# Performance work log

Measured on AMD Instinct MI355X. Metric: run time of the kernel, lower is better.

## Reference

```python
import jax, jax.numpy as jnp
import numpy as np
from math import sqrt

GAMMA = 2.0       # init gamma
SIGMA_G = 1.0     # init sigma (Gaussian prior width) -- NOT the forward `sigma` arg
ALPHA = 0.1       # prior mixing weight


def _hilbert_filter(L, dtype):
    h = np.zeros(L, dtype=np.float32)
    if L % 2 == 0:
        h[0] = h[L // 2] = 1.0
        h[1:L // 2] = 2.0
    else:
        h[0] = 1.0
        h[1:(L + 1) // 2] = 2.0
    return jnp.asarray(h)


def setup_inputs() -> dict:
    key = jax.random.key(0)
    ks = jax.random.split(key, 6)
    B, L, H, E = 4, 1024, 8, 64
    return {
        "q": jax.random.normal(ks[0], (B, L, H, E), jnp.float32),
        "k": jax.random.normal(ks[1], (B, L, H, E), jnp.float32),
        "v": jax.random.normal(ks[2], (B, L, H, E), jnp.float32),
        "sigma": jax.random.normal(ks[3], (B, L, H), jnp.float32),
        "hurst": jax.random.normal(ks[4], (B, L, H), jnpp if False else jnp.float32) if False else jax.random.normal(ks[4], (B, L, H), jnp.float32),
        "tau": jax.random.normal(ks[5], (B, L, H), jnp.float32),
    }


def reference(q, k, v, sigma, hurst, tau):
    B, L, H, E = q.shape
    scale = 1.0 / sqrt(E)

    # QK scores [B,H,L,L]. Note: original calls scores.masked_fill (non-inplace,
    # result discarded), so the causal mask has NO effect -- reproduced faithfully.
    scores = jnp.einsum('blhe,bshe->bhls', q, k)
    attn = scale * scores

    hurst_t = jax.nn.sigmoid(hurst) * 0.99 + 0.01          # [B,L,H]
    tau_t = jax.nn.sigmoid(tau) * 0.9 + 0.1                # [B,L,H]

    # fractal abscissa -> Gaussian prior [B,H,L,L]
    psi = jnp.cumsum(jnp.exp(GAMMA * hurst_t), axis=1)     # [B,L,H]
    diff = psi[:, :, None, :] - psi[:, None, :, :]          # [B,L,L,H]
    prior = jnp.exp(-diff ** 2 / (2.0 * SIGMA_G ** 2))
    prior = jnp.transpose(prior, (0, 3, 1, 2))              # [B,H,L,L]
    prior = prior / (jnp.sum(prior, axis=-1, keepdims=True) + 1e-6)

    # phase gate from Hilbert analytic signal of q-features
    x = jnp.transpose(q, (0, 2, 1, 3)).reshape(B, L, H * E)  # [B,L,C]
    sig = jnp.transpose(x, (0, 2, 1))                         # [B,C,L]
    hfilt = _hilbert_filter(L, sig.dtype)
    analytic = jnp.fft.ifft(jnp.fft.fft(sig, axis=-1) * hfilt[None, None, :], axis=-1)
    phase = jnp.arctan2(jnp.imag(analytic), jnp.real(analytic))  # [B,C,L]
    theta = jnp.arctan2(jnp.mean(jnp.sin(phase), axis=1),
                        jnp.mean(jnp.cos(phase), axis=1))        # [B,L]
    dphi = jnp.sin(0.5 * (theta[:, :, None] - theta[:, None, :]))  # [B,L,L]
    tau_d = jax.lax.stop_gradient(tau_t)                     # tau is detached
    S = jnp.exp(-dphi[..., None] ** 2 / (2.0 * tau_d[:, :, None, :] ** 2))  # [B,L,L,H]
    gate = jnp.transpose(S, (0, 3, 1, 2))                    # [B,H,L,L]

    prior = prior * gate
    prior = prior / (jnp.sum(prior, axis=-1, keepdims=True) + 1e-6)

    series = jax.nn.softmax(attn, axis=-1)                   # dropout p=0
    attn_combined = (1.0 - ALPHA) * series + ALPHA * prior
    V = jnp.einsum('bhls,bshd->blhd', attn_combined, v)      # [B,L,H,E]
    return V
```

## Files before the change

kernel.cpp:

```cpp
#include <hip/hip_runtime.h>
#include <hip/hip_bf16.h>
#include <math.h>

#define LL 1024
#define BB 4
#define HH 8
#define EE 64
#define CC (HH*EE)

typedef __attribute__((ext_vector_type(4))) float f32x4;
typedef __attribute__((ext_vector_type(8))) short bf16x8;
typedef __attribute__((ext_vector_type(4))) short bf16x4;

__device__ __forceinline__ unsigned short f2bf(float x) {
    unsigned u = __float_as_uint(x);
    u += 0x7FFFu + ((u >> 16) & 1u);
    return (unsigned short)(u >> 16);
}

__device__ __forceinline__ void dma16(const void* g, void* l) {
    typedef const __attribute__((address_space(1))) unsigned int* gup;
    typedef __attribute__((address_space(3))) unsigned int* lup;
    gup gp = (gup)(unsigned long long)g;
    lup lp = (lup)(unsigned int)(unsigned long long)l;
    __builtin_amdgcn_global_load_lds(gp, lp, 16, 0, 0);
}

__global__ __launch_bounds__(1024) void k_pre1(const float* __restrict__ hurst,
                                               const float* __restrict__ tau,
                                               const float* __restrict__ q,
                                               const float* __restrict__ kk,
                                               const float* __restrict__ vv,
                                               float* __restrict__ psi,
                                               float* __restrict__ taut,
                                               unsigned short* __restrict__ Agh,
                                               unsigned short* __restrict__ Agl,
                                               unsigned short* __restrict__ Xh,
                                               unsigned short* __restrict__ Xl,
                                               unsigned short* __restrict__ Qp,
                                               unsigned short* __restrict__ Kp,
                                               unsigned short* __restrict__ Vp) {
    __shared__ __align__(16) char smem[32768];
    int bid = blockIdx.x;
    int t = threadIdx.x;

    if (bid < 32) {
        float* sh = (float*)smem;
        int bh = bid;
        int b = bh >> 3, h = bh & 7;
        int l = t;
        float hu = hurst[((size_t)b * LL + l) * HH + h];
        float ht = 1.f / (1.f + expf(-hu)) * 0.99f + 0.01f;
        sh[l] = expf(2.0f * ht);
        __syncthreads();
        for (int off = 1; off < LL; off <<= 1) {
            float tmp = (l >= off) ? sh[l - off] : 0.f;
            __syncthreads();
            sh[l] += tmp;
            __syncthreads();
        }
        psi[((size_t)b * HH + h) * LL + l] = sh[l];
        float tv = tau[((size_t)b * LL + l) * HH + h];
        taut[((size_t)b * HH + h) * LL + l] = 1.f / (1.f + expf(-tv)) * 0.9f + 0.1f;
    } else if (bid < 288) {
        float* sh = (float*)smem;
        {
            int d = t;
            float vvv = 0.f;
            if (d & 1) {
                float a = 3.14159265358979323846f * (float)d / (float)LL;
                vvv = (2.0f / (float)LL) * (cosf(a) / sinf(a));
            }
            sh[d] = vvv;
        }
        __syncthreads();
        int bb = bid - 32;
        int im = bb >> 4, kt = bb & 15;
        if (t < 512) {
            int row = t >> 3, gr = t & 7;
            int i = im * 64 + row;
            bf16x8 hv, lv;
            #pragma unroll
            for (int j = 0; j < 8; ++j) {
                int kl = gr * 8 + j;
                float gg = sh[(i - kt * 64 - kl) & 1023];
                unsigned short hh = f2bf(gg);
                hv[j] = (short)hh;
                lv[j] = (short)f2bf(gg - __uint_as_float(((unsigned)hh) << 16));
            }
            size_t base = (size_t)bb * 4096;
            int pos = gr ^ (row & 7);
            *(bf16x8*)&Agh[base + row * 64 + pos * 8] = hv;
            *(bf16x8*)&Agl[base + row * 64 + pos * 8] = lv;
        }
    } else if (bid < 544) {
        int bb = bid - 288;
        int kt = bb >> 4, np = bb & 15;
        int bq = np >> 2;
        const float* qb = q + (size_t)bq * LL * CC;
        size_t base = (size_t)bb * 8192;
        int gid = t;
        int nl = gid & 15, nb = (gid >> 4) & 7, kg = gid >> 7;
        int e_n = np * 128 + nb * 16 + nl;
        int cy = (e_n >> 6) & 7;
        int e = e_n & 63;
        bf16x8 hv, lv;
        #pragma unroll
        for (int j = 0; j < 8; ++j) {
            int k2 = kt * 64 + kg * 8 + j;
            int l = ((k2 & 127) << 3) | cy;
            int h2 = k2 >> 7;
            float val = qb[l * 512 + h2 * 64 + e];
            unsigned short hh = f2bf(val);
            hv[j] = (short)hh;
            lv[j] = (short)f2bf(val - __uint_as_float(((unsigned)hh) << 16));
        }
        *(bf16x8*)&Xh[base + (size_t)gid * 8] = hv;
        *(bf16x8*)&Xl[base + (size_t)gid * 8] = lv;
    } else {
        int bb = bid - 544;
        int sub = t >> 8, tt = t & 255;
        int blk = bb * 4 + sub;
        int tile = blk & 15;
        int bh = blk >> 4;
        int h = bh & 7, b = bh >> 3;
        int l0 = tile * 64;
        unsigned short* vt = (unsigned short*)smem + sub * 4096;

        const float* qg = q + ((size_t)(b * LL + l0) * CC + (size_t)h * EE);
        const float* kg = kk + ((size_t)(b * LL + l0) * CC + (size_t)h * EE);
        const float* vg = vv + ((size_t)(b * LL + l0) * CC + (size_t)h * EE);
        unsigned short* Qo = Qp + ((size_t)bh * LL + l0) * 64;
        unsigned short* Ko = Kp + ((size_t)bh * LL + l0) * 64;
        unsigned short* Vo = Vp + ((size_t)bh * 16 + tile) * 4096;

        const float QS = 0.18033688011112042f;

        #pragma unroll
        for (int it = 0; it < 2; ++it) {
            int x = it * 256 + tt;
            int row = x >> 3, gr = x & 7;
            int pos = (gr ^ (row & 7)) * 8;
            const float* src = qg + (size_t)row * CC + gr * 8;
            float4 a4 = *(const float4*)src;
            float4 b4 = *(const float4*)(src + 4);
            bf16x8 o;
            o[0] = (short)f2bf(QS * a4.x); o[1] = (short)f2bf(QS * a4.y);
            o[2] = (short)f2bf(QS * a4.z); o[3] = (short)f2bf(QS * a4.w);
            o[4] = (short)f2bf(QS * b4.x); o[5] = (short)f2bf(QS * b4.y);
            o[6] = (short)f2bf(QS * b4.z); o[7] = (short)f2bf(QS * b4.w);
            *(bf16x8*)&Qo[row * 64 + pos] = o;
            src = kg + (size_t)row * CC + gr * 8;
            a4 = *(const float4*)src;
            b4 = *(const float4*)(src + 4);
            o[0] = (short)f2bf(a4.x); o[1] = (short)f2bf(a4.y);
            o[2] = (short)f2bf(a4.z); o[3] = (short)f2bf(a4.w);
            o[4] = (short)f2bf(b4.x); o[5] = (short)f2bf(b4.y);
            o[6] = (short)f2bf(b4.z); o[7] = (short)f2bf(b4.w);
            *(bf16x8*)&Ko[row * 64 + pos] = o;
        }

        #pragma unroll
        for (int it = 0; it < 4; ++it) {
            int x = it * 256 + tt;
            int s = x >> 4, i = x & 15;
            float4 a4 = *(const float4*)(vg + (size_t)s * CC + i * 4);
            int c = s >> 5, g4 = (s >> 2) & 3;
            int jj = ((s >> 4) & 1) * 4 + (s & 3);
            float vals[4] = {a4.x, a4.y, a4.z, a4.w};
            #pragma unroll
            for (int j2 = 0; j2 < 4; ++j2) {
                int e = i * 4 + j2;
                int ef = e >> 4, m16 = e & 15;
                vt[((((ef * 2 + c) * 4 + g4) * 16 + m16) * 8) + jj] = f2bf(vals[j2]);
            }
        }
        __syncthreads();
        #pragma unroll
        for (int it = 0; it < 2; ++it) {
            int x = it * 256 + tt;
            *(bf16x8*)&Vo[x * 8] = *(bf16x8*)&vt[x * 8];
        }
    }
}

__global__ __launch_bounds__(256) void k_hilb(const float* __restrict__ q,
                                              const unsigned short* __restrict__ Agh,
                                              const unsigned short* __restrict__ Agl,
                                              const unsigned short* __restrict__ Xh,
                                              const unsigned short* __restrict__ Xl,
                                              float* __restrict__ part_s,
                                              float* __restrict__ part_c) {
    __shared__ __align__(16) char smemB[98304];

    int t = threadIdx.x, lid = t & 63, wv = t >> 6;
    int m16 = lid & 15, g = lid >> 4;
    int wi = wv >> 1, wn = wv & 1;

    int bid = blockIdx.x;
    int xcd = bid & 7, o = bid >> 3;
    int im = ((xcd >> 2) << 3) + (o & 7);
    int np = ((xcd & 3) << 2) + (o >> 3);
    int i0 = im * 64, n0 = np * 128;
    int bq = np >> 2, quad = np & 3;
    const float* qb = q + (size_t)bq * LL * CC;

    const char* Ah_g = (const char*)Agh + (size_t)im * 16 * 8192;
    const char* Al_g = (const char*)Agl + (size_t)im * 16 * 8192;
    const char* Xh_g = (const char*)Xh;
    const char* Xl_g = (const char*)Xl;

#define AHOFF(bf) ((bf) * 49152)
#define ALOFF(bf) ((bf) * 49152 + 8192)
#define XHOFF(bf) ((bf) * 49152 + 16384)
#define XLOFF(bf) ((bf) * 49152 + 32768)
#define STAGE(bf, kt)                                                          \
    {                                                                          \
        size_t xb = ((size_t)(kt) * 16 + np) * 16384;                          \
        _Pragma("unroll")                                                      \
        for (int c = 0; c < 2; ++c) {                                          \
            int ch = wv + 4 * c;                                               \
            dma16(Ah_g + (kt) * 8192 + ch * 1024 + lid * 16,                   \
                  smemB + AHOFF(bf) + ch * 1024);                              \
            dma16(Al_g + (kt) * 8192 + ch * 1024 + lid * 16,                   \
                  smemB + ALOFF(bf) + ch * 1024);                              \
        }                                                                      \
        _Pragma("unroll")                                                      \
        for (int c = 0; c < 4; ++c) {                                          \
            int ch = wv + 4 * c;                                               \
            dma16(Xh_g + xb + ch * 1024 + lid * 16,                            \
                  smemB + XHOFF(bf) + ch * 1024);                              \
            dma16(Xl_g + xb + ch * 1024 + lid * 16,                            \
                  smemB + XLOFF(bf) + ch * 1024);                              \
        }                                                                      \
    }

    STAGE(0, 0);
    __syncthreads();

    f32x4 acc[2][4];
    #pragma unroll
    for (int mf = 0; mf < 2; ++mf)
        #pragma unroll
        for (int nf = 0; nf < 4; ++nf) acc[mf][nf] = (f32x4){0.f, 0.f, 0.f, 0.f};

    int cur = 0;
    for (int kt = 0; kt < 16; ++kt) {
        if (kt < 15) {
            STAGE(cur ^ 1, kt + 1);
            asm volatile("s_waitcnt vmcnt(12)" ::: "memory");
        } else {
            asm volatile("s_waitcnt vmcnt(0)" ::: "memory");
        }
        __builtin_amdgcn_sched_barrier(0);
        __builtin_amdgcn_s_barrier();
        asm volatile("" ::: "memory");

        const unsigned short* AhL = (const unsigned short*)(smemB + AHOFF(cur));
        const unsigned short* AlL = (const unsigned short*)(smemB + ALOFF(cur));
        const unsigned short* XhL = (const unsigned short*)(smemB + XHOFF(cur));
        const unsigned short* XlL = (const unsigned short*)(smemB + XLOFF(cur));

        __builtin_amdgcn_s_setprio(1);
        #pragma unroll
        for (int s = 0; s < 2; ++s) {
            bf16x8 Ahf[2], Alf[2];
            #pragma unroll
            for (int mf = 0; mf < 2; ++mf) {
                int row = wi * 32 + 16 * mf + m16;
                int pos = (s * 4 + g) ^ (m16 & 7);
                Ahf[mf] = *(bf16x8*)&AhL[row * 64 + pos * 8];
                Alf[mf] = *(bf16x8*)&AlL[row * 64 + pos * 8];
            }
            #pragma unroll
            for (int nf = 0; nf < 4; ++nf) {
                int nb = wn * 4 + nf;
                int goff = (((s * 4 + g) * 8 + nb) * 16 + m16) * 8;
                bf16x8 Bh = *(bf16x8*)&XhL[goff];
                bf16x8 Bl = *(bf16x8*)&XlL[goff];
                #pragma unroll
                for (int mf = 0; mf < 2; ++mf) {
                    acc[mf][nf] = __builtin_amdgcn_mfma_f32_16x16x32_bf16(Ahf[mf], Bh, acc[mf][nf], 0, 0, 0);
                    acc[mf][nf] = __builtin_amdgcn_mfma_f32_16x16x32_bf16(Ahf[mf], Bl, acc[mf][nf], 0, 0, 0);
                    acc[mf][nf] = __builtin_amdgcn_mfma_f32_16x16x32_bf16(Alf[mf], Bh, acc[mf][nf], 0, 0, 0);
                }
            }
        }
        __builtin_amdgcn_s_setprio(0);

        asm volatile("" ::: "memory");
        __builtin_amdgcn_s_barrier();
        cur ^= 1;
    }

    float svacc[2][4], cvacc[2][4];
    #pragma unroll
    for (int mf = 0; mf < 2; ++mf)
        #pragma unroll
        for (int r = 0; r < 4; ++r) { svacc[mf][r] = 0.f; cvacc[mf][r] = 0.f; }

    #pragma unroll
    for (int mf = 0; mf < 2; ++mf) {
        #pragma unroll
        for (int nf = 0; nf < 4; ++nf) {
            #pragma unroll
            for (int r = 0; r < 4; ++r) {
                float iv = acc[mf][nf][r];
                int ig = i0 + wi * 32 + 16 * mf + 4 * g + r;
                int ng = n0 + wn * 64 + 16 * nf + m16;
                int cc2 = ng & 511;
                int cy = cc2 >> 6, e = cc2 & 63;
                int l = ((ig & 127) << 3) | cy;
                int h2 = ig >> 7;
                float re = qb[l * 512 + h2 * 64 + e];
                float rr = sqrtf(re * re + iv * iv);
                float sv, cv;
                if (rr > 0.f) { sv = iv / rr; cv = re / rr; }
                else { sv = 0.f; cv = 1.f; }
                svacc[mf][r] += sv;
                cvacc[mf][r] += cv;
            }
        }
    }
    __syncthreads();
    float* psv = (float*)smemB;
    float* pcv = (float*)(smemB + 512);
    #pragma unroll
    for (int mf = 0; mf < 2; ++mf) {
        #pragma unroll
        for (int r = 0; r < 4; ++r) {
            float s = svacc[mf][r], c = cvacc[mf][r];
            s += __shfl_xor(s, 1); s += __shfl_xor(s, 2);
            s += __shfl_xor(s, 4); s += __shfl_xor(s, 8);
            c += __shfl_xor(c, 1); c += __shfl_xor(c, 2);
            c += __shfl_xor(c, 4); c += __shfl_xor(c, 8);
            if (m16 == 0) {
                psv[wv * 32 + 16 * mf + 4 * g + r] = s;
                pcv[wv * 32 + 16 * mf + 4 * g + r] = c;
            }
        }
    }
    __syncthreads();
    if (t < 64) {
        int wg = (t >> 5) * 2;
        float s = psv[wg * 32 + (t & 31)] + psv[(wg + 1) * 32 + (t & 31)];
        float c = pcv[wg * 32 + (t & 31)] + pcv[(wg + 1) * 32 + (t & 31)];
        size_t oidx = ((size_t)bq * 1024 + (i0 + t)) * 4 + quad;
        part_s[oidx] = s;
        part_c[oidx] = c;
    }
#undef AHOFF
#undef ALOFF
#undef XHOFF
#undef XLOFF
#undef STAGE
}

__global__ __launch_bounds__(1024) void k_pcs(const float* __restrict__ psi,
                                              const float* __restrict__ taut,
                                              const float* __restrict__ part_s,
                                              const float* __restrict__ part_c,
                                              float* __restrict__ pcs) {
    int tid = blockIdx.x * 1024 + threadIdx.x;
    int bh = tid >> 10, l = tid & 1023;
    int b = bh >> 3;
    float ss = 0.f, cc2 = 0.f;
    size_t pbase = ((size_t)b * 1024 + l) * 4;
    #pragma unroll
    for (int qd = 0; qd < 4; ++qd) {
        ss += part_s[pbase + qd];
        cc2 += part_c[pbase + qd];
    }
    float r2 = ss * ss + cc2 * cc2;
    float cth = 1.f, sth = 0.f;
    if (r2 > 0.f) {
        float rn = rsqrtf(r2);
        cth = cc2 * rn; sth = ss * rn;
    }
    float ta = taut[tid];
    float4 o;
    o.x = psi[tid] * 0.8493218003f;
    o.y = cth;
    o.z = sth;
    o.w = 0.3606737602f / (ta * ta);
    *(float4*)&pcs[(size_t)tid * 4] = o;
}

__global__ __launch_bounds__(256, 3) void k_attn(const unsigned short* __restrict__ Qp,
                                                 const unsigned short* __restrict__ Kp,
                                                 const unsigned short* __restrict__ Vp,
                                                 const float* __restrict__ pcs,
                                                 float* __restrict__ out) {
    __shared__ __align__(16) char smemB[43008];

    int t = threadIdx.x;
    int lid = t & 63;
    int wv = t >> 6;
    int m16 = lid & 15;
    int g = lid >> 4;

    int bid = blockIdx.x;
    int blk = (bid & 7) * 64 + (bid >> 3);
    int qt = blk & 15;
    int bh = blk >> 4;
    int h = bh & 7, b = bh >> 3;
    int l0 = qt * 64;

    const char* Qg = (const char*)(Qp + ((size_t)bh * LL + l0) * 64);
    const char* Kg = (const char*)(Kp + (size_t)bh * LL * 64);
    const char* Vg = (const char*)(Vp + (size_t)bh * LL * 64);
    const float* pcsg = pcs + (size_t)bh * LL * 4;

    int qrow = wv * 16 + m16;
    float4 myq = *(const float4*)&pcsg[(size_t)(l0 + qrow) * 4];
    float psiq = myq.x, cq = myq.y, sq = myq.z;
    float wgt = myq.w, nwgt = -myq.w;

#define KOFF(bf) (8192 + (bf) * 8192)
#define VOFF(bf) (24576 + (bf) * 8192)
#define POFF(bf) (40960 + (bf) * 1024)
#define STAGE(bf, tile)                                                        \
    {                                                                          \
        const char* kb8 = Kg + (tile) * 8192;                                  \
        const char* vb8 = Vg + (tile) * 8192;                                  \
        _Pragma("unroll")                                                      \
        for (int c = 0; c < 2; ++c) {                                          \
            int ch = wv + 4 * c;                                               \
            dma16(kb8 + ch * 1024 + lid * 16, smemB + KOFF(bf) + ch * 1024);   \
            dma16(vb8 + ch * 1024 + lid * 16, smemB + VOFF(bf) + ch * 1024);   \
        }                                                                      \
        dma16((const char*)pcsg + (tile) * 1024 + lid * 16, smemB + POFF(bf)); \
    }

    #pragma unroll
    for (int c = 0; c < 2; ++c) {
        int ch = wv + 4 * c;
        dma16(Qg + ch * 1024 + lid * 16, smemB + ch * 1024);
    }
    STAGE(0, 0);
    __syncthreads();

    const unsigned short* qlds = (const unsigned short*)smemB;
    bf16x8 qf[2];
    #pragma unroll
    for (int ec = 0; ec < 2; ++ec) {
        int pos = (4 * ec + g) ^ (m16 & 7);
        qf[ec] = *(bf16x8*)&qlds[(wv * 16 + m16) * 64 + pos * 8];
    }

    f32x4 accS[4], accP[4];
    #pragma unroll
    for (int f = 0; f < 4; ++f) {
        accS[f] = (f32x4){0.f, 0.f, 0.f, 0.f};
        accP[f] = (f32x4){0.f, 0.f, 0.f, 0.f};
    }
    float ssel = 0.f, spgl = 0.f;
    int cur = 0;

    for (int tile = 0; tile < 16; ++tile) {
        if (tile < 15) {
            STAGE(cur ^ 1, tile + 1);
            asm volatile("s_waitcnt vmcnt(5)" ::: "memory");
        } else {
            asm volatile("s_waitcnt vmcnt(0)" ::: "memory");
        }
        __builtin_amdgcn_sched_barrier(0);
        __builtin_amdgcn_s_barrier();
        asm volatile("" ::: "memory");

        const unsigned short* kbuf = (const unsigned short*)(smemB + KOFF(cur));
        const unsigned short* vbuf = (const unsigned short*)(smemB + VOFF(cur));
        const float* pcb = (const float*)(smemB + POFF(cur));

        f32x4 st[4];
        #pragma unroll
        for (int f = 0; f < 4; ++f) st[f] = (f32x4){0.f, 0.f, 0.f, 0.f};
        __builtin_amdgcn_s_setprio(1);
        #pragma unroll
        for (int ec = 0; ec < 2; ++ec) {
            int pos = (4 * ec + g) ^ (m16 & 7);
            #pragma unroll
            for (int f = 0; f < 4; ++f) {
                bf16x8 ka = *(bf16x8*)&kbuf[(16 * f + m16) * 64 + pos * 8];
                st[f] = __builtin_amdgcn_mfma_f32_16x16x32_bf16(ka, qf[ec], st[f], 0, 0, 0);
            }
        }
        __builtin_amdgcn_s_setprio(0);

        float psum = 0.f;
        float ps_[16], pg_[16];
        #pragma unroll
        for (int f = 0; f < 4; ++f) {
            #pragma unroll
            for (int r = 0; r < 4; ++r) {
                float4 pc4 = *(const float4*)&pcb[(16 * f + 4 * g + r) * 4];
                float p = exp2f(st[f][r]);
                psum += p;
                float d = psiq - pc4.x;
                float cd = fmaf(cq, pc4.y, sq * pc4.z);
                float arg = fmaf(-d, d, fmaf(wgt, cd, nwgt));
                float pgv = exp2f(arg);
                spgl += pgv;
                ps_[f * 4 + r] = p;
                pg_[f * 4 + r] = pgv;
            }
        }
        ssel += psum;

        union PK8 { unsigned w[8]; bf16x8 v[2]; } SS, GG;
        #pragma unroll
        for (int i2 = 0; i2 < 8; ++i2) {
            __hip_bfloat162 hs = __float22bfloat162_rn(
                make_float2(ps_[2 * i2], ps_[2 * i2 + 1]));
            __hip_bfloat162 hg = __float22bfloat162_rn(
                make_float2(pg_[2 * i2], pg_[2 * i2 + 1]));
            unsigned ws2, wg2;
            __builtin_memcpy(&ws2, &hs, 4);
            __builtin_memcpy(&wg2, &hg, 4);
            SS.w[i2] = ws2;
            GG.w[i2] = wg2;
        }

        __builtin_amdgcn_s_setprio(1);
        #pragma unroll
        for (int c = 0; c < 2; ++c) {
            #pragma unroll
            for (int ef = 0; ef < 4; ++ef) {
                bf16x8 vb = *(bf16x8*)&vbuf[(((ef * 2 + c) * 4 + g) * 16 + m16) * 8];
                accS[ef] = __builtin_amdgcn_mfma_f32_16x16x32_bf16(SS.v[c], vb, accS[ef], 0, 0, 0);
                accP[ef] = __builtin_amdgcn_mfma_f32_16x16x32_bf16(GG.v[c], vb, accP[ef], 0, 0, 0);
            }
        }
        __builtin_amdgcn_s_setprio(0);

        asm volatile("" ::: "memory");
        __builtin_amdgcn_s_barrier();
        cur ^= 1;
    }

    ssel += __shfl_xor(ssel, 16); ssel += __shfl_xor(ssel, 32);
    spgl += __shfl_xor(spgl, 16); spgl += __shfl_xor(spgl, 32);
    float cs = 0.9f / ssel;
    float cp = 0.1f / (spgl + 1e-6f);
    float* ob = out + ((size_t)(b * LL + l0 + wv * 16) * CC + (size_t)h * EE);
    #pragma unroll
    for (int r = 0; r < 4; ++r) {
        float csr = __shfl(cs, 4 * g + r);
        float cpr = __shfl(cp, 4 * g + r);
        #pragma unroll
        for (int f = 0; f < 4; ++f) {
            ob[(size_t)(4 * g + r) * CC + 16 * f + m16] =
                csr * accS[f][r] + cpr * accP[f][r];
        }
    }
#undef KOFF
#undef VOFF
#undef POFF
#undef STAGE
}

extern "C" void kernel_launch(void* const* d_in, const int* in_sizes, int n_in,
                              void* d_out, int out_size, void* d_ws, size_t ws_size,
                              hipStream_t stream) {
    const float* q = (const float*)d_in[0];
    const float* k = (const float*)d_in[1];
    const float* v = (const float*)d_in[2];
    const float* hurst = (const float*)d_in[4];
    const float* tau = (const float*)d_in[5];
    float* out = (float*)d_out;

    float* ws = (float*)d_ws;
    float* gi     = ws;
    float* psi    = gi + LL;
    float* taut   = psi + (size_t)BB * HH * LL;
    float* costh  = taut + (size_t)BB * HH * LL;
    float* sinth  = costh + (size_t)BB * LL;
    float* part_s = sinth + (size_t)BB * LL;
    float* part_c = part_s + (size_t)BB * LL * 4;
    float* pcs    = part_c + (size_t)BB * LL * 4;
    unsigned short* Qp = (unsigned short*)(pcs + (size_t)BB * HH * LL * 4);
    unsigned short* Kp = Qp + (size_t)BB * HH * LL * 64;
    unsigned short* Vp = Kp + (size_t)BB * HH * LL * 64;
    unsigned short* Agh = Vp + (size_t)BB * HH * LL * 64;
    unsigned short* Agl = Agh + (size_t)1048576;
    unsigned short* Xh  = (unsigned short*)d_out;
    unsigned short* Xl  = Xh + (size_t)2097152;

    k_pre1<<<672, 1024, 0, stream>>>(hurst, tau, q, k, v, psi, taut,
                                     Agh, Agl, Xh, Xl, Qp, Kp, Vp);
    k_hilb<<<256, 256, 0, stream>>>(q, Agh, Agl, Xh, Xl, part_s, part_c);
    k_pcs<<<32, 1024, 0, stream>>>(psi, taut, part_s, part_c, pcs);
    k_attn<<<BB * HH * (LL / 64), 256, 0, stream>>>(Qp, Kp, Vp, pcs, out);
}
```

Baseline: 80.32 us.

## Halve Hilbert GEMM N-tile to double grid, and stage two key tiles per attention step

The Hilbert DFT GEMM kernel now uses 64-column output tiles instead of 128, launching 512 blocks with smaller shared buffers so more of the GPU is occupied. Its partial sin/cos sums are split eight ways instead of four, and the reduction kernel reads eight partials. The attention kernel now stages 128 keys per pipeline step (two 64-key subtiles), halving barrier and wait overhead. It also loads Q fragments straight from global memory into registers and drops the occupancy hint. The larger shared-memory footprint may lower attention occupancy, and the Hilbert A-matrix is loaded twice as often across blocks.

```diff
diff --git a/kernel.cpp b/kernel.cpp
--- a/kernel.cpp
+++ b/kernel.cpp
@@ -191,7 +191,7 @@
                                               const unsigned short* __restrict__ Xl,
                                               float* __restrict__ part_s,
                                               float* __restrict__ part_c) {
-    __shared__ __align__(16) char smemB[98304];
+    __shared__ __align__(16) char smemB[65536];
 
     int t = threadIdx.x, lid = t & 63, wv = t >> 6;
     int m16 = lid & 15, g = lid >> 4;
@@ -199,10 +199,11 @@
 
     int bid = blockIdx.x;
     int xcd = bid & 7, o = bid >> 3;
-    int im = ((xcd >> 2) << 3) + (o & 7);
-    int np = ((xcd & 3) << 2) + (o >> 3);
-    int i0 = im * 64, n0 = np * 128;
-    int bq = np >> 2, quad = np & 3;
+    int im  = ((xcd >> 2) << 3) + (o & 7);
+    int np8 = ((xcd & 3) << 3) + (o >> 3);
+    int i0 = im * 64, n0 = np8 * 64;
+    int bq = np8 >> 3, oct = np8 & 7;
+    int np = np8 >> 1, nb0 = (np8 & 1) * 4;
     const float* qb = q + (size_t)bq * LL * CC;
 
     const char* Ah_g = (const char*)Agh + (size_t)im * 16 * 8192;
@@ -210,10 +211,10 @@
     const char* Xh_g = (const char*)Xh;
     const char* Xl_g = (const char*)Xl;
 
-#define AHOFF(bf) ((bf) * 49152)
-#define ALOFF(bf) ((bf) * 49152 + 8192)
-#define XHOFF(bf) ((bf) * 49152 + 16384)
-#define XLOFF(bf) ((bf) * 49152 + 32768)
+#define AHOFF(bf) ((bf) * 32768)
+#define ALOFF(bf) ((bf) * 32768 + 8192)
+#define XHOFF(bf) ((bf) * 32768 + 16384)
+#define XLOFF(bf) ((bf) * 32768 + 24576)
 #define STAGE(bf, kt)                                                          \
     {                                                                          \
         size_t xb = ((size_t)(kt) * 16 + np) * 16384;                          \
@@ -224,13 +225,9 @@
                   smemB + AHOFF(bf) + ch * 1024);                              \
             dma16(Al_g + (kt) * 8192 + ch * 1024 + lid * 16,                   \
                   smemB + ALOFF(bf) + ch * 1024);                              \
-        }                                                                      \
-        _Pragma("unroll")                                                      \
-        for (int c = 0; c < 4; ++c) {                                          \
-            int ch = wv + 4 * c;                                               \
-            dma16(Xh_g + xb + ch * 1024 + lid * 16,                            \
+            dma16(Xh_g + xb + (ch * 8 + nb0) * 256 + lid * 16,                 \
                   smemB + XHOFF(bf) + ch * 1024);                              \
-            dma16(Xl_g + xb + ch * 1024 + lid * 16,                            \
+            dma16(Xl_g + xb + (ch * 8 + nb0) * 256 + lid * 16,                 \
                   smemB + XLOFF(bf) + ch * 1024);                              \
         }                                                                      \
     }
@@ -238,17 +235,17 @@
     STAGE(0, 0);
     __syncthreads();
 
-    f32x4 acc[2][4];
+    f32x4 acc[2][2];
     #pragma unroll
     for (int mf = 0; mf < 2; ++mf)
         #pragma unroll
-        for (int nf = 0; nf < 4; ++nf) acc[mf][nf] = (f32x4){0.f, 0.f, 0.f, 0.f};
+        for (int nf = 0; nf < 2; ++nf) acc[mf][nf] = (f32x4){0.f, 0.f, 0.f, 0.f};
 
     int cur = 0;
     for (int kt = 0; kt < 16; ++kt) {
         if (kt < 15) {
             STAGE(cur ^ 1, kt + 1);
-            asm volatile("s_waitcnt vmcnt(12)" ::: "memory");
+            asm volatile("s_waitcnt vmcnt(8)" ::: "memory");
         } else {
             asm volatile("s_waitcnt vmcnt(0)" ::: "memory");
         }
@@ -273,9 +270,9 @@
                 Alf[mf] = *(bf16x8*)&AlL[row * 64 + pos * 8];
             }
             #pragma unroll
-            for (int nf = 0; nf < 4; ++nf) {
-                int nb = wn * 4 + nf;
-                int goff = (((s * 4 + g) * 8 + nb) * 16 + m16) * 8;
+            for (int nf = 0; nf < 2; ++nf) {
+                int nbl = wn * 2 + nf;
+                int goff = (((s * 4 + g) * 4 + nbl) * 16 + m16) * 8;
                 bf16x8 Bh = *(bf16x8*)&XhL[goff];
                 bf16x8 Bl = *(bf16x8*)&XlL[goff];
                 #pragma unroll
@@ -302,12 +299,12 @@
     #pragma unroll
     for (int mf = 0; mf < 2; ++mf) {
         #pragma unroll
-        for (int nf = 0; nf < 4; ++nf) {
+        for (int nf = 0; nf < 2; ++nf) {
             #pragma unroll
             for (int r = 0; r < 4; ++r) {
                 float iv = acc[mf][nf][r];
                 int ig = i0 + wi * 32 + 16 * mf + 4 * g + r;
-                int ng = n0 + wn * 64 + 16 * nf + m16;
+                int ng = n0 + (wn * 2 + nf) * 16 + m16;
                 int cc2 = ng & 511;
                 int cy = cc2 >> 6, e = cc2 & 63;
                 int l = ((ig & 127) << 3) | cy;
@@ -345,7 +342,7 @@
         int wg = (t >> 5) * 2;
         float s = psv[wg * 32 + (t & 31)] + psv[(wg + 1) * 32 + (t & 31)];
         float c = pcv[wg * 32 + (t & 31)] + pcv[(wg + 1) * 32 + (t & 31)];
-        size_t oidx = ((size_t)bq * 1024 + (i0 + t)) * 4 + quad;
+        size_t oidx = ((size_t)bq * 1024 + (i0 + t)) * 8 + oct;
         part_s[oidx] = s;
         part_c[oidx] = c;
     }
@@ -365,9 +362,9 @@
     int bh = tid >> 10, l = tid & 1023;
     int b = bh >> 3;
     float ss = 0.f, cc2 = 0.f;
-    size_t pbase = ((size_t)b * 1024 + l) * 4;
-    #pragma unroll
-    for (int qd = 0; qd < 4; ++qd) {
+    size_t pbase = ((size_t)b * 1024 + l) * 8;
+    #pragma unroll
+    for (int qd = 0; qd < 8; ++qd) {
         ss += part_s[pbase + qd];
         cc2 += part_c[pbase + qd];
     }
@@ -386,12 +383,12 @@
     *(float4*)&pcs[(size_t)tid * 4] = o;
 }
 
-__global__ __launch_bounds__(256, 3) void k_attn(const unsigned short* __restrict__ Qp,
-                                                 const unsigned short* __restrict__ Kp,
-                                                 const unsigned short* __restrict__ Vp,
-                                                 const float* __restrict__ pcs,
-                                                 float* __restrict__ out) {
-    __shared__ __align__(16) char smemB[43008];
+__global__ __launch_bounds__(256) void k_attn(const unsigned short* __restrict__ Qp,
+                                              const unsigned short* __restrict__ Kp,
+                                              const unsigned short* __restrict__ Vp,
+                                              const float* __restrict__ pcs,
+                                              float* __restrict__ out) {
+    __shared__ __align__(16) char smemB[69632];
 
     int t = threadIdx.x;
     int lid = t & 63;
@@ -416,37 +413,31 @@
     float psiq = myq.x, cq = myq.y, sq = myq.z;
     float wgt = myq.w, nwgt = -myq.w;
 
-#define KOFF(bf) (8192 + (bf) * 8192)
-#define VOFF(bf) (24576 + (bf) * 8192)
-#define POFF(bf) (40960 + (bf) * 1024)
-#define STAGE(bf, tile)                                                        \
+#define KOFF(bf) ((bf) * 16384)
+#define VOFF(bf) (32768 + (bf) * 16384)
+#define POFF(bf) (65536 + (bf) * 2048)
+#define STAGE(bf, it)                                                          \
     {                                                                          \
-        const char* kb8 = Kg + (tile) * 8192;                                  \
-        const char* vb8 = Vg + (tile) * 8192;                                  \
+        const char* kb8 = Kg + (it) * 16384;                                   \
+        const char* vb8 = Vg + (it) * 16384;                                   \
         _Pragma("unroll")                                                      \
-        for (int c = 0; c < 2; ++c) {                                          \
+        for (int c = 0; c < 4; ++c) {                                          \
             int ch = wv + 4 * c;                                               \
             dma16(kb8 + ch * 1024 + lid * 16, smemB + KOFF(bf) + ch * 1024);   \
             dma16(vb8 + ch * 1024 + lid * 16, smemB + VOFF(bf) + ch * 1024);   \
         }                                                                      \
-        dma16((const char*)pcsg + (tile) * 1024 + lid * 16, smemB + POFF(bf)); \
-    }
-
-    #pragma unroll
-    for (int c = 0; c < 2; ++c) {
-        int ch = wv + 4 * c;
-        dma16(Qg + ch * 1024 + lid * 16, smemB + ch * 1024);
+        dma16((const char*)pcsg + (it) * 2048 + (wv & 1) * 1024 + lid * 16,    \
+              smemB + POFF(bf) + (wv & 1) * 1024);                             \
+    }
+
+    bf16x8 qf[2];
+    #pragma unroll
+    for (int ec = 0; ec < 2; ++ec) {
+        int pos = (4 * ec + g) ^ (m16 & 7);
+        qf[ec] = *(const bf16x8*)(Qg + ((wv * 16 + m16) * 64 + pos * 8) * 2);
     }
     STAGE(0, 0);
     __syncthreads();
-
-    const unsigned short* qlds = (const unsigned short*)smemB;
-    bf16x8 qf[2];
-    #pragma unroll
-    for (int ec = 0; ec < 2; ++ec) {
-        int pos = (4 * ec + g) ^ (m16 & 7);
-        qf[ec] = *(bf16x8*)&qlds[(wv * 16 + m16) * 64 + pos * 8];
-    }
 
     f32x4 accS[4], accP[4];
     #pragma unroll
@@ -457,10 +448,10 @@
     float ssel = 0.f, spgl = 0.f;
     int cur = 0;
 
-    for (int tile = 0; tile < 16; ++tile) {
-        if (tile < 15) {
-            STAGE(cur ^ 1, tile + 1);
-            asm volatile("s_waitcnt vmcnt(5)" ::: "memory");
+    for (int it = 0; it < 8; ++it) {
+        if (it < 7) {
+            STAGE(cur ^ 1, it + 1);
+            asm volatile("s_waitcnt vmcnt(9)" ::: "memory");
         } else {
             asm volatile("s_waitcnt vmcnt(0)" ::: "memory");
         }
@@ -468,70 +459,73 @@
         __builtin_amdgcn_s_barrier();
         asm volatile("" ::: "memory");
 
-        const unsigned short* kbuf = (const unsigned short*)(smemB + KOFF(cur));
-        const unsigned short* vbuf = (const unsigned short*)(smemB + VOFF(cur));
-        const float* pcb = (const float*)(smemB + POFF(cur));
-
-        f32x4 st[4];
-        #pragma unroll
-        for (int f = 0; f < 4; ++f) st[f] = (f32x4){0.f, 0.f, 0.f, 0.f};
-        __builtin_amdgcn_s_setprio(1);
-        #pragma unroll
-        for (int ec = 0; ec < 2; ++ec) {
-            int pos = (4 * ec + g) ^ (m16 & 7);
+        #pragma unroll
+        for (int t2 = 0; t2 < 2; ++t2) {
+            const unsigned short* kbuf = (const unsigned short*)(smemB + KOFF(cur) + t2 * 8192);
+            const unsigned short* vbuf = (const unsigned short*)(smemB + VOFF(cur) + t2 * 8192);
+            const float* pcb = (const float*)(smemB + POFF(cur) + t2 * 1024);
+
+            f32x4 st[4];
+            #pragma unroll
+            for (int f = 0; f < 4; ++f) st[f] = (f32x4){0.f, 0.f, 0.f, 0.f};
+            __builtin_amdgcn_s_setprio(1);
+            #pragma unroll
+            for (int ec = 0; ec < 2; ++ec) {
+                int pos = (4 * ec + g) ^ (m16 & 7);
+                #pragma unroll
+                for (int f = 0; f < 4; ++f) {
+                    bf16x8 ka = *(bf16x8*)&kbuf[(16 * f + m16) * 64 + pos * 8];
+                    st[f] = __builtin_amdgcn_mfma_f32_16x16x32_bf16(ka, qf[ec], st[f], 0, 0, 0);
+                }
+            }
+            __builtin_amdgcn_s_setprio(0);
+
+            float psum = 0.f;
+            float ps_[16], pg_[16];
             #pragma unroll
             for (int f = 0; f < 4; ++f) {
-                bf16x8 ka = *(bf16x8*)&kbuf[(16 * f + m16) * 64 + pos * 8];
-                st[f] = __builtin_amdgcn_mfma_f32_16x16x32_bf16(ka, qf[ec], st[f], 0, 0, 0);
-            }
-        }
-        __builtin_amdgcn_s_setprio(0);
-
-        float psum = 0.f;
-        float ps_[16], pg_[16];
-        #pragma unroll
-        for (int f = 0; f < 4; ++f) {
-            #pragma unroll
-            for (int r = 0; r < 4; ++r) {
-                float4 pc4 = *(const float4*)&pcb[(16 * f + 4 * g + r) * 4];
-                float p = exp2f(st[f][r]);
-                psum += p;
-                float d = psiq - pc4.x;
-                float cd = fmaf(cq, pc4.y, sq * pc4.z);
-                float arg = fmaf(-d, d, fmaf(wgt, cd, nwgt));
-                float pgv = exp2f(arg);
-                spgl += pgv;
-                ps_[f * 4 + r] = p;
-                pg_[f * 4 + r] = pgv;
-            }
-        }
-        ssel += psum;
-
-        union PK8 { unsigned w[8]; bf16x8 v[2]; } SS, GG;
-        #pragma unroll
-        for (int i2 = 0; i2 < 8; ++i2) {
-            __hip_bfloat162 hs = __float22bfloat162_rn(
-                make_float2(ps_[2 * i2], ps_[2 * i2 + 1]));
-            __hip_bfloat162 hg = __float22bfloat162_rn(
-                make_float2(pg_[2 * i2], pg_[2 * i2 + 1]));
-            unsigned ws2, wg2;
-            __builtin_memcpy(&ws2, &hs, 4);
-            __builtin_memcpy(&wg2, &hg, 4);
-            SS.w[i2] = ws2;
-            GG.w[i2] = wg2;
-        }
-
-        __builtin_amdgcn_s_setprio(1);
-        #pragma unroll
-        for (int c = 0; c < 2; ++c) {
-            #pragma unroll
-            for (int ef = 0; ef < 4; ++ef) {
-                bf16x8 vb = *(bf16x8*)&vbuf[(((ef * 2 + c) * 4 + g) * 16 + m16) * 8];
-                accS[ef] = __builtin_amdgcn_mfma_f32_16x16x32_bf16(SS.v[c], vb, accS[ef], 0, 0, 0);
-                accP[ef] = __builtin_amdgcn_mfma_f32_16x16x32_bf16(GG.v[c], vb, accP[ef], 0, 0, 0);
-            }
-        }
-        __builtin_amdgcn_s_setprio(0);
+                #pragma unroll
+                for (int r = 0; r < 4; ++r) {
+                    float4 pc4 = *(const float4*)&pcb[(16 * f + 4 * g + r) * 4];
+                    float p = exp2f(st[f][r]);
+                    psum += p;
+                    float d = psiq - pc4.x;
+                    float cd = fmaf(cq, pc4.y, sq * pc4.z);
+                    float arg = fmaf(-d, d, fmaf(wgt, cd, nwgt));
+                    float pgv = exp2f(arg);
+                    spgl += pgv;
+                    ps_[f * 4 + r] = p;
+                    pg_[f * 4 + r] = pgv;
+                }
+            }
+            ssel += psum;
+
+            union PK8 { unsigned w[8]; bf16x8 v[2]; } SS, GG;
+            #pragma unroll
+            for (int i2 = 0; i2 < 8; ++i2) {
+                __hip_bfloat162 hs = __float22bfloat162_rn(
+                    make_float2(ps_[2 * i2], ps_[2 * i2 + 1]));
+                __hip_bfloat162 hg = __float22bfloat162_rn(
+                    make_float2(pg_[2 * i2], pg_[2 * i2 + 1]));
+                unsigned ws2, wg2;
+                __builtin_memcpy(&ws2, &hs, 4);
+                __builtin_memcpy(&wg2, &hg, 4);
+                SS.w[i2] = ws2;
+                GG.w[i2] = wg2;
+            }
+
+            __builtin_amdgcn_s_setprio(1);
+            #pragma unroll
+            for (int c = 0; c < 2; ++c) {
+                #pragma unroll
+                for (int ef = 0; ef < 4; ++ef) {
+                    bf16x8 vb = *(bf16x8*)&vbuf[(((ef * 2 + c) * 4 + g) * 16 + m16) * 8];
+                    accS[ef] = __builtin_amdgcn_mfma_f32_16x16x32_bf16(SS.v[c], vb, accS[ef], 0, 0, 0);
+                    accP[ef] = __builtin_amdgcn_mfma_f32_16x16x32_bf16(GG.v[c], vb, accP[ef], 0, 0, 0);
+                }
+            }
+            __builtin_amdgcn_s_setprio(0);
+        }
 
         asm volatile("" ::: "memory");
         __builtin_amdgcn_s_barrier();
@@ -570,25 +564,22 @@
     float* out = (float*)d_out;
 
     float* ws = (float*)d_ws;
-    float* gi     = ws;
-    float* psi    = gi + LL;
-    float* taut   = psi + (size_t)BB * HH * LL;
-    float* costh  = taut + (size_t)BB * HH * LL;
-    float* sinth  = costh + (size_t)BB * LL;
-    float* part_s = sinth + (size_t)BB * LL;
-    float* part_c = part_s + (size_t)BB * LL * 4;
-    float* pcs    = part_c + (size_t)BB * LL * 4;
-    unsigned short* Qp = (unsigned short*)(pcs + (size_t)BB * HH * LL * 4);
-    unsigned short* Kp = Qp + (size_t)BB * HH * LL * 64;
-    unsigned short* Vp = Kp + (size_t)BB * HH * LL * 64;
-    unsigned short* Agh = Vp + (size_t)BB * HH * LL * 64;
+    float* psi    = ws;
+    float* taut   = psi + 32768;
+    float* part_s = taut + 32768;
+    float* part_c = part_s + 32768;
+    float* pcs    = part_c + 32768;
+    unsigned short* Qp = (unsigned short*)(pcs + 131072);
+    unsigned short* Kp = Qp + (size_t)2097152;
+    unsigned short* Vp = Kp + (size_t)2097152;
+    unsigned short* Agh = Vp + (size_t)2097152;
     unsigned short* Agl = Agh + (size_t)1048576;
     unsigned short* Xh  = (unsigned short*)d_out;
     unsigned short* Xl  = Xh + (size_t)2097152;
 
     k_pre1<<<672, 1024, 0, stream>>>(hurst, tau, q, k, v, psi, taut,
                                      Agh, Agl, Xh, Xl, Qp, Kp, Vp);
-    k_hilb<<<256, 256, 0, stream>>>(q, Agh, Agl, Xh, Xl, part_s, part_c);
+    k_hilb<<<512, 256, 0, stream>>>(q, Agh, Agl, Xh, Xl, part_s, part_c);
     k_pcs<<<32, 1024, 0, stream>>>(psi, taut, part_s, part_c, pcs);
     k_attn<<<BB * HH * (LL / 64), 256, 0, stream>>>(Qp, Kp, Vp, pcs, out);
 }
```

Measured after the change: 75.30 us, median of 2. -6.2%, faster.
